# Optimization experiments

Measured on AMD Instinct MI355X. Metric: run time of the kernel, lower is better.

Reference implementation:

```python
import jax, jax.numpy as jnp
import numpy as np

DIM = 1024
HEADS = 16
HEAD_DIM = DIM // HEADS
SCALE = HEAD_DIM ** -0.5


def apply_rope(x, theta=10000.0):
    # x: [b, h, n, d]
    n, d = x.shape[2], x.shape[3]
    seq = jnp.arange(n, dtype=jnp.float32)
    inv = 1.0 / (theta ** (jnp.arange(0, d, 2, dtype=jnp.float32) / d))  # [d/2]
    freqs = seq[:, None] * inv[None, :]  # [n, d/2]
    cos = jnp.cos(freqs)[None, None]  # [1,1,n,d/2]
    sin = jnp.sin(freqs)[None, None]
    x1, x2 = jnp.split(x, 2, axis=-1)
    return jnp.concatenate([x1 * cos - x2 * sin, x1 * sin + x2 * cos], axis=-1)


def setup_inputs() -> dict:
    key = jax.random.key(0)
    ks = jax.random.split(key, 7)
    s = DIM ** -0.5
    return {
        "x": jax.random.normal(ks[0], (2, 2048, DIM), dtype=jnp.float32),
        "Wqkv": jax.random.normal(ks[1], (3 * DIM, DIM), dtype=jnp.float32) * s,
        "bqkv": jax.random.normal(ks[2], (3 * DIM,), dtype=jnp.float32) * 0.02,
        "Wpre": jax.random.normal(ks[3], (HEADS, HEADS), dtype=jnp.float32) * HEADS ** -0.5,
        "Wpost": jax.random.normal(ks[4], (HEADS, HEADS), dtype=jnp.float32) * HEADS ** -0.5,
        "Wout": jax.random.normal(ks[5], (DIM, DIM), dtype=jnp.float32) * s,
        "bout": jax.random.normal(ks[6], (DIM,), dtype=jnp.float32) * 0.02,
    }


def reference(x, Wqkv, bqkv, Wpre, Wpost, Wout, bout):
    b, n, _ = x.shape
    qkv = x @ Wqkv.T + bqkv  # [b, n, 3*dim]
    q, k, v = jnp.split(qkv, 3, axis=-1)
    # [b, n, dim] -> [b, h, n, d]
    reshape = lambda t: t.reshape(b, n, HEADS, HEAD_DIM).transpose(0, 2, 1, 3)
    q, k, v = reshape(q), reshape(k), reshape(v)
    q = apply_rope(q)
    k = apply_rope(k)
    logits = jnp.einsum('bhid,bhjd->bhij', q, k) * SCALE
    # pre-softmax talking heads: Linear(heads->heads), y[...,g] = sum_h x[...,h] * Wpre[g,h]
    logits = jnp.einsum('bhij,gh->bgij', logits, Wpre)
    attn = jax.nn.softmax(logits, axis=-1)
    attn = jnp.einsum('bhij,gh->bgij', attn, Wpost)
    out = jnp.einsum('bhij,bhjd->bhid', attn, v)
    out = out.transpose(0, 2, 1, 3).reshape(b, n, DIM)
    return out @ Wout.T + bout
```

## Files before the change

### kernel.cpp

```cpp
#include <hip/hip_runtime.h>
#include <cstddef>
#include <cstdint>

#define SEQ    2048
#define DMODEL 1024
#define NHEAD  16
#define HDIM   64
#define SCALE  0.125f
#define LOG2E  1.4426950408889634f

typedef _Float16 f16;
typedef unsigned short u16;
typedef unsigned int   u32;
typedef __attribute__((ext_vector_type(8))) _Float16 h8v;
typedef __attribute__((ext_vector_type(4))) _Float16 h4v;
typedef __attribute__((ext_vector_type(4))) float    f4v;

__device__ __forceinline__ u32 pkh(float a, float b) {
    u16 x = __builtin_bit_cast(u16, (f16)a);
    u16 y = __builtin_bit_cast(u16, (f16)b);
    return (u32)x | ((u32)y << 16);
}

__device__ __forceinline__ float fexp2(float x) {
#if __has_builtin(__builtin_amdgcn_exp2f)
    return __builtin_amdgcn_exp2f(x);
#else
    return exp2f(x);
#endif
}

__device__ __forceinline__ f4v mfma32(h8v a, h8v b, f4v c) {
    return __builtin_amdgcn_mfma_f32_16x16x32_f16(a, b, c, 0, 0, 0);
}
__device__ __forceinline__ f4v mfma16(h4v a, h4v b, f4v c) {
    return __builtin_amdgcn_mfma_f32_16x16x16f16(a, b, c, 0, 0, 0);
}

__global__ __launch_bounds__(256)
void rope_tab_kernel(float2* __restrict__ tab)
{
    int gid = blockIdx.x * 256 + threadIdx.x;
    int pos = gid >> 5, t = gid & 31;
    float inv = exp2f((float)(-2 * t) * (0.015625f * 13.287712379549449f));
    float c, s;
    sincosf((float)pos * inv, &s, &c);
    tab[gid] = make_float2(c, s);
}

__global__ __launch_bounds__(256)
void cvt_f16_kernel(const float* __restrict__ x, const float* __restrict__ Wqkv,
                    const float* __restrict__ Wout,
                    f16* __restrict__ Xh, f16* __restrict__ Wqh, f16* __restrict__ Woh)
{
    size_t i = ((size_t)blockIdx.x * 256 + threadIdx.x) * 8;
    const float* src; f16* dst; size_t off;
    if (i < 4194304)      { src = x;    dst = Xh;  off = i; }
    else if (i < 7340032) { src = Wqkv; dst = Wqh; off = i - 4194304; }
    else                  { src = Wout; dst = Woh; off = i - 7340032; }
    float4 a = *(const float4*)&src[off];
    float4 b = *(const float4*)&src[off + 4];
    uint4 o;
    o.x = pkh(a.x, a.y); o.y = pkh(a.z, a.w);
    o.z = pkh(b.x, b.y); o.w = pkh(b.z, b.w);
    *(uint4*)&dst[off] = o;
}

__global__ __launch_bounds__(256)
void gemm_f16_kernel(const f16* __restrict__ A, const f16* __restrict__ B,
                     const float* __restrict__ bias, void* __restrict__ Cout,
                     int N, int K, int mode)
{
    __shared__ __align__(16) char Asb[8192];
    __shared__ __align__(16) char Bsb[8192];
    int tid = threadIdx.x;
    int w = tid >> 6, l = tid & 63, lr = l & 15, lc = l >> 4;
    int row0 = blockIdx.y * 128, col0 = blockIdx.x * 128;
    int wr = (w >> 1) * 64, wc = (w & 1) * 64;

    f4v acc[4][4];
    #pragma unroll
    for (int m = 0; m < 4; ++m)
        #pragma unroll
        for (int n = 0; n < 4; ++n) acc[m][n] = (f4v){0.f, 0.f, 0.f, 0.f};

    int r0 = tid >> 2, k0s = tid & 3;
    int r1 = (tid + 256) >> 2, k1s = tid & 3;

    uint4 ra0, ra1, rb0, rb1;
    ra0 = *(const uint4*)&A[(size_t)(row0 + r0) * K + k0s * 8];
    ra1 = *(const uint4*)&A[(size_t)(row0 + r1) * K + k1s * 8];
    rb0 = *(const uint4*)&B[(size_t)(col0 + r0) * K + k0s * 8];
    rb1 = *(const uint4*)&B[(size_t)(col0 + r1) * K + k1s * 8];

    int NT = K >> 5;
    for (int kt = 0; kt < NT; ++kt) {
        *(uint4*)(Asb + r0 * 64 + ((k0s ^ (r0 & 3)) << 4)) = ra0;
        *(uint4*)(Asb + r1 * 64 + ((k1s ^ (r1 & 3)) << 4)) = ra1;
        *(uint4*)(Bsb + r0 * 64 + ((k0s ^ (r0 & 3)) << 4)) = rb0;
        *(uint4*)(Bsb + r1 * 64 + ((k1s ^ (r1 & 3)) << 4)) = rb1;
        if (kt + 1 < NT) {
            int kk = (kt + 1) * 32;
            ra0 = *(const uint4*)&A[(size_t)(row0 + r0) * K + kk + k0s * 8];
            ra1 = *(const uint4*)&A[(size_t)(row0 + r1) * K + kk + k1s * 8];
            rb0 = *(const uint4*)&B[(size_t)(col0 + r0) * K + kk + k0s * 8];
            rb1 = *(const uint4*)&B[(size_t)(col0 + r1) * K + kk + k1s * 8];
        }
        __syncthreads();
        h8v af[4], bf[4];
        #pragma unroll
        for (int m = 0; m < 4; ++m) {
            int row = wr + m * 16 + lr;
            af[m] = *(h8v*)(Asb + row * 64 + ((lc ^ (row & 3)) << 4));
        }
        #pragma unroll
        for (int n = 0; n < 4; ++n) {
            int col = wc + n * 16 + lr;
            bf[n] = *(h8v*)(Bsb + col * 64 + ((lc ^ (col & 3)) << 4));
        }
        #pragma unroll
        for (int m = 0; m < 4; ++m)
            #pragma unroll
            for (int n = 0; n < 4; ++n)
                acc[m][n] = mfma32(af[m], bf[n], acc[m][n]);
        __syncthreads();
    }

    #pragma unroll
    for (int m = 0; m < 4; ++m)
        #pragma unroll
        for (int r = 0; r < 4; ++r) {
            int row = row0 + wr + m * 16 + lc * 4 + r;
            #pragma unroll
            for (int n = 0; n < 4; ++n) {
                int col = col0 + wc + n * 16 + lr;
                float v = acc[m][n][r] + bias[col];
                if (mode == 0) ((f16*)Cout)[(size_t)row * N + col] = (f16)v;
                else           ((float*)Cout)[(size_t)row * N + col] = v;
            }
        }
}

__global__ __launch_bounds__(256)
void pack_qk_kernel(const f16* __restrict__ QKVh, const float2* __restrict__ tab,
                    f16* __restrict__ Qh, f16* __restrict__ Kh)
{
    int gid = blockIdx.x * 256 + threadIdx.x;
    int i     = gid & 15;
    int t8    = (gid >> 4) & 3;
    int h     = (gid >> 6) & 15;
    int rh    = (gid >> 10) & 255;
    int which = (gid >> 18) & 1;
    int row = rh * 16 + i;
    int pos = row & (SEQ - 1);
    int b   = row >> 11;
    f16* dst = which ? Kh : Qh;

    h8v x1 = *(const h8v*)&QKVh[(size_t)row * 3072 + which * 1024 + h * 64 + t8 * 8];
    h8v x2 = *(const h8v*)&QKVh[(size_t)row * 3072 + which * 1024 + h * 64 + t8 * 8 + 32];

    float y1[8], y2[8];
    #pragma unroll
    for (int e = 0; e < 8; ++e) {
        int t = t8 * 8 + e;
        float2 cs = tab[pos * 32 + t];
        float a1 = (float)x1[e], a2 = (float)x2[e];
        y1[e] = a1 * cs.x - a2 * cs.y;
        y2[e] = a1 * cs.y + a2 * cs.x;
    }
    int it = pos >> 4;
    size_t b0 = (((((size_t)(b*128 + it)*16 + h)*2 + 0)*4 + t8)*16 + i)*8;
    size_t b1 = (((((size_t)(b*128 + it)*16 + h)*2 + 1)*4 + t8)*16 + i)*8;
    uint4 o0, o1;
    o0.x = pkh(y1[0], y1[1]); o0.y = pkh(y1[2], y1[3]);
    o0.z = pkh(y1[4], y1[5]); o0.w = pkh(y1[6], y1[7]);
    o1.x = pkh(y2[0], y2[1]); o1.y = pkh(y2[2], y2[3]);
    o1.z = pkh(y2[4], y2[5]); o1.w = pkh(y2[6], y2[7]);
    *(uint4*)(dst + b0) = o0;
    *(uint4*)(dst + b1) = o1;
}

__global__ __launch_bounds__(256)
void pack_v_kernel(const f16* __restrict__ QKVh, f16* __restrict__ Vt)
{
    int gid = blockIdx.x * 256 + threadIdx.x;
    int dd = gid & 15;
    int jc = (gid >> 4) & 3;
    int dt = (gid >> 6) & 3;
    int g  = (gid >> 8) & 15;
    int jt = (gid >> 12) & 63;
    int b  = (gid >> 18) & 1;
    int d = g * 64 + dt * 16 + dd;
    f16 v[8];
    #pragma unroll
    for (int e = 0; e < 8; ++e) {
        int j = jt * 32 + jc * 8 + e;
        v[e] = QKVh[(size_t)(b * SEQ + j) * 3072 + 2048 + d];
    }
    size_t off = ((((((size_t)b*64 + jt)*16 + g)*4 + dt)*4 + jc)*16 + dd)*8;
    uint4 o;
    o.x = pkh((float)v[0], (float)v[1]); o.y = pkh((float)v[2], (float)v[3]);
    o.z = pkh((float)v[4], (float)v[5]); o.w = pkh((float)v[6], (float)v[7]);
    *(uint4*)(Vt + off) = o;
}

__global__ __launch_bounds__(256)
void pack_ctx_kernel(const f16* __restrict__ Cp, f16* __restrict__ Ch)
{
    size_t i = ((size_t)blockIdx.x * 256 + threadIdx.x) * 8;
    h8v p0 = *(const h8v*)&Cp[i];
    h8v p1 = *(const h8v*)&Cp[i + 4194304];
    float s[8];
    #pragma unroll
    for (int e = 0; e < 8; ++e)
        s[e] = (float)p0[e] + (float)p1[e];
    uint4 o;
    o.x = pkh(s[0], s[1]); o.y = pkh(s[2], s[3]);
    o.z = pkh(s[4], s[5]); o.w = pkh(s[6], s[7]);
    *(uint4*)&Ch[i] = o;
}

template<int FULL>
__global__ __launch_bounds__(1024, FULL ? 1 : 2)
void attn_core(const f16* __restrict__ Qh, const f16* __restrict__ Kh,
               const f16* __restrict__ Vt, const float* __restrict__ Wpre,
               const float* __restrict__ Wpost, const float* __restrict__ Zp,
               float* __restrict__ Zout, f16* __restrict__ Octx)
{
    __shared__ __align__(16) char ss[65536];
    __shared__ __align__(16) char es[FULL ? 65536 : 16];

    int tid = threadIdx.x;
    int wv = tid >> 6;
    int l  = tid & 63;
    int lr = l & 15;
    int lc = l >> 4;

    int bid   = blockIdx.x;
    int it2   = bid & 63;
    int b     = (bid >> 6) & 1;
    int split = bid >> 7;

    h4v wpre4;
    #pragma unroll
    for (int e = 0; e < 4; ++e) wpre4[e] = (f16)(Wpre[lr * 16 + lc * 4 + e] * (SCALE * LOG2E));
    h4v wpost;
    if (FULL) {
        #pragma unroll
        for (int e = 0; e < 4; ++e) wpost[e] = (f16)Wpost[lr * 16 + lc * 4 + e];
    }

    h8v qf[2][2];
    #pragma unroll
    for (int itl = 0; itl < 2; ++itl)
        #pragma unroll
        for (int ks = 0; ks < 2; ++ks) {
            size_t off = ((((size_t)((b*128 + it2*2 + itl)*16 + wv)*2 + ks)*4 + lc)*16 + lr)*8;
            qf[itl][ks] = *(const h8v*)(Qh + off);
        }

    f4v m4n[2];
    if (FULL) {
        float* zrd = (float*)ss;
        if (tid < 512) {
            int itl = tid >> 8, g = (tid >> 4) & 15, i = tid & 15;
            size_t idx = (size_t)(b * 16 + g) * SEQ + it2 * 32 + itl * 16 + i;
            zrd[tid] = log2f(Zp[idx] + Zp[65536 + idx] + Zp[131072 + idx] + Zp[196608 + idx]);
        }
        __syncthreads();
        #pragma unroll
        for (int itl = 0; itl < 2; ++itl)
            #pragma unroll
            for (int r = 0; r < 4; ++r)
                m4n[itl][r] = -zrd[itl * 256 + (lc * 4 + r) * 16 + lr];
        __syncthreads();
    }

    f4v pv[2][4];
    if (FULL) {
        #pragma unroll
        for (int itl = 0; itl < 2; ++itl)
            #pragma unroll
            for (int dt = 0; dt < 4; ++dt) pv[itl][dt] = (f4v){0.f, 0.f, 0.f, 0.f};
    }
    float zacc[2][4] = {};

    const int NSTEP = FULL ? 16 : 8;
    int j0beg = split * (FULL ? 1024 : 512);
    int jtbeg = j0beg >> 4;
    int jvbeg = j0beg >> 5;

    for (int s = 0; s < NSTEP; ++s) {
        h8v vf0[4];
        if (FULL) {
            int jt32 = jvbeg + s * 2;
            #pragma unroll
            for (int dt = 0; dt < 4; ++dt) {
                size_t voff = (((((size_t)(b*64 + jt32)*16 + wv)*4 + dt)*4 + lc)*16 + lr)*8;
                vf0[dt] = *(const h8v*)(Vt + voff);
            }
        }
        #pragma unroll
        for (int jsp = 0; jsp < 2; ++jsp) {
            h8v kf[2][2];
            #pragma unroll
            for (int js2 = 0; js2 < 2; ++js2)
                #pragma unroll
                for (int ks = 0; ks < 2; ++ks) {
                    int jt = jtbeg + s * 4 + jsp * 2 + js2;
                    size_t off = ((((size_t)((b*128 + jt)*16 + wv)*2 + ks)*4 + lc)*16 + lr)*8;
                    kf[js2][ks] = *(const h8v*)(Kh + off);
                }
            #pragma unroll
            for (int itl = 0; itl < 2; ++itl)
                #pragma unroll
                for (int js2 = 0; js2 < 2; ++js2) {
                    f4v q = (f4v){0.f, 0.f, 0.f, 0.f};
                    q = mfma32(qf[itl][0], kf[js2][0], q);
                    q = mfma32(qf[itl][1], kf[js2][1], q);
                    int js = jsp * 2 + js2;
                    #pragma unroll
                    for (int r = 0; r < 4; ++r) {
                        int i = lc * 4 + r;
                        int addr = itl * 32768 + ((wv >> 2) * 4 + js) * 2048
                                 + i * 128 + ((lr ^ i) << 3) + (wv & 3) * 2;
                        *(u16*)(ss + addr) = __builtin_bit_cast(u16, (f16)q[r]);
                    }
                }
        }
        __syncthreads();

        #pragma unroll
        for (int itl = 0; itl < 2; ++itl) {
            u32 a2p[4][2];
            #pragma unroll
            for (int tt = 0; tt < 4; ++tt) {
                int t = wv * 4 + tt;
                int addr = itl * 32768 + (lc * 4 + (t >> 4)) * 2048
                         + lr * 128 + (((t & 15) ^ lr) << 3);
                union { uint2 u; h4v v; } cv;
                cv.u = *(uint2*)(ss + addr);
                if (!FULL) {
                    f4v s1 = mfma16(wpre4, cv.v, (f4v){0.f, 0.f, 0.f, 0.f});
                    #pragma unroll
                    for (int r = 0; r < 4; ++r) zacc[itl][r] += fexp2(s1[r]);
                } else {
                    f4v s1 = mfma16(wpre4, cv.v, m4n[itl]);
                    h4v pf;
                    #pragma unroll
                    for (int r = 0; r < 4; ++r) pf[r] = (f16)fexp2(s1[r]);
                    f4v a2 = mfma16(wpost, pf, (f4v){0.f, 0.f, 0.f, 0.f});
                    #pragma unroll
                    for (int r = 0; r < 4; ++r) {
                        u32 v = (u32)__builtin_bit_cast(u16, (f16)a2[r]);
                        if (tt & 1) a2p[r][tt >> 1] |= v << 16;
                        else        a2p[r][tt >> 1]  = v;
                    }
                }
            }
            if (FULL) {
                #pragma unroll
                for (int r = 0; r < 4; ++r) {
                    int gq = lc * 4 + r;
                    int off = itl * 32768 + gq * 2048 + lr * 128
                            + ((wv * 8) ^ ((lr & 7) << 4));
                    *(uint2*)(es + off) = make_uint2(a2p[r][0], a2p[r][1]);
                }
            }
        }
        h8v vf1[4];
        if (FULL) {
            int jt32 = jvbeg + s * 2 + 1;
            #pragma unroll
            for (int dt = 0; dt < 4; ++dt) {
                size_t voff = (((((size_t)(b*64 + jt32)*16 + wv)*4 + dt)*4 + lc)*16 + lr)*8;
                vf1[dt] = *(const h8v*)(Vt + voff);
            }
        }
        __syncthreads();

        if (FULL) {
            #pragma unroll
            for (int itl = 0; itl < 2; ++itl) {
                h8v af0 = *(h8v*)(es + itl * 32768 + wv * 2048 + lr * 128
                                  + ((0 * 64 + lc * 16) ^ ((lr & 7) << 4)));
                h8v af1 = *(h8v*)(es + itl * 32768 + wv * 2048 + lr * 128
                                  + ((1 * 64 + lc * 16) ^ ((lr & 7) << 4)));
                #pragma unroll
                for (int dt = 0; dt < 4; ++dt)
                    pv[itl][dt] = mfma32(af0, vf0[dt], pv[itl][dt]);
                #pragma unroll
                for (int dt = 0; dt < 4; ++dt)
                    pv[itl][dt] = mfma32(af1, vf1[dt], pv[itl][dt]);
            }
        }
    }

    if (!FULL) {
        float* zrd = (float*)ss;
        #pragma unroll
        for (int itl = 0; itl < 2; ++itl)
            #pragma unroll
            for (int r = 0; r < 4; ++r)
                zrd[itl * 4096 + ((lc * 4 + r) * 16 + lr) * 16 + wv] = zacc[itl][r];
        __syncthreads();
        if (tid < 512) {
            int itl = tid >> 8, gi = tid & 255;
            float z = 0.f;
            #pragma unroll
            for (int w2 = 0; w2 < 16; ++w2) z += zrd[itl * 4096 + gi * 16 + w2];
            int g = gi >> 4, i = gi & 15;
            Zout[(size_t)split * 65536 + (size_t)(b * 16 + g) * SEQ + it2 * 32 + itl * 16 + i] = z;
        }
    } else {
        f16* dst = Octx + (size_t)split * 4194304;
        #pragma unroll
        for (int itl = 0; itl < 2; ++itl)
            #pragma unroll
            for (int dt = 0; dt < 4; ++dt)
                #pragma unroll
                for (int r = 0; r < 4; ++r) {
                    int row = it2 * 32 + itl * 16 + lc * 4 + r;
                    int col = wv * 64 + dt * 16 + lr;
                    dst[(size_t)(b * SEQ + row) * DMODEL + col] = (f16)pv[itl][dt][r];
                }
    }
}

extern "C" void kernel_launch(void* const* d_in, const int* in_sizes, int n_in,
                              void* d_out, int out_size, void* d_ws, size_t ws_size,
                              hipStream_t stream)
{
    const float* x     = (const float*)d_in[0];
    const float* Wqkv  = (const float*)d_in[1];
    const float* bqkv  = (const float*)d_in[2];
    const float* Wpre  = (const float*)d_in[3];
    const float* Wpost = (const float*)d_in[4];
    const float* Wout  = (const float*)d_in[5];
    const float* bout  = (const float*)d_in[6];
    float* out = (float*)d_out;

    float* ws = (float*)d_ws;
    f16*   QKVh = (f16*)(ws);
    f16*   CTXp = (f16*)(ws);
    f16*   Xh   = (f16*)(ws + 8388608);
    f16*   Wqh  = (f16*)(ws + 10485760);
    f16*   Woh  = (f16*)(ws + 12058624);
    f16*   Qh   = (f16*)(ws + 12582912);
    f16*   Kh   = (f16*)(ws + 14680064);
    f16*   Vt   = (f16*)(ws + 16777216);
    f16*   Ch   = (f16*)(ws + 18874368);
    float* Zp   = ws + 19922944;
    float2* Tab = (float2*)(ws + 20185088);

    dim3 blk(256);
    rope_tab_kernel<<<256, blk, 0, stream>>>(Tab);
    cvt_f16_kernel<<<4096, blk, 0, stream>>>(x, Wqkv, Wout, Xh, Wqh, Woh);
    gemm_f16_kernel<<<dim3(24, 32), blk, 0, stream>>>(Xh, Wqh, bqkv, (void*)QKVh, 3072, 1024, 0);
    pack_qk_kernel<<<2048, blk, 0, stream>>>(QKVh, Tab, Qh, Kh);
    pack_v_kernel<<<2048, blk, 0, stream>>>(QKVh, Vt);
    attn_core<0><<<512, dim3(1024), 0, stream>>>(Qh, Kh, Vt, Wpre, Wpost, nullptr, Zp, nullptr);
    attn_core<1><<<256, dim3(1024), 0, stream>>>(Qh, Kh, Vt, Wpre, Wpost, Zp, nullptr, CTXp);
    pack_ctx_kernel<<<2048, blk, 0, stream>>>(CTXp, Ch);
    gemm_f16_kernel<<<dim3(8, 32), blk, 0, stream>>>(Ch, Woh, bout, (void*)out, 1024, 1024, 1);
}
```

Before: 209.5 us.

## Use direct global-to-LDS loads in GEMM and prefetch K fragments in attention

The GEMM now uses global_load_lds to stream A/B tiles straight into shared memory, replacing the register-staged load-and-store path, and issues the next tile's loads after the second barrier. The attention kernel loads the second half of the K fragments before computing scores and, in the full pass, prefetches the next step's first K fragments across the barrier. The aim is to hide global load latency and cut register and VGPR-to-LDS traffic. The GEMM loses its register double buffering, so next-tile loads now land during the barrier rather than overlapping the MFMA loop, and the LDS layout depends on how global_load_lds places each wave's 64 lanes.

```diff
diff --git a/kernel.cpp b/kernel.cpp
--- a/kernel.cpp
+++ b/kernel.cpp
@@ -36,6 +36,10 @@
 __device__ __forceinline__ f4v mfma16(h4v a, h4v b, f4v c) {
     return __builtin_amdgcn_mfma_f32_16x16x16f16(a, b, c, 0, 0, 0);
 }
+
+#define GLD16(src, dst) __builtin_amdgcn_global_load_lds(                    \
+        (const __attribute__((address_space(1))) void*)(src),                \
+        (__attribute__((address_space(3))) void*)(dst), 16, 0, 0)
 
 __global__ __launch_bounds__(256)
 void rope_tab_kernel(float2* __restrict__ tab)
@@ -84,28 +88,25 @@
         #pragma unroll
         for (int n = 0; n < 4; ++n) acc[m][n] = (f4v){0.f, 0.f, 0.f, 0.f};
 
-    int r0 = tid >> 2, k0s = tid & 3;
-    int r1 = (tid + 256) >> 2, k1s = tid & 3;
-
-    uint4 ra0, ra1, rb0, rb1;
-    ra0 = *(const uint4*)&A[(size_t)(row0 + r0) * K + k0s * 8];
-    ra1 = *(const uint4*)&A[(size_t)(row0 + r1) * K + k1s * 8];
-    rb0 = *(const uint4*)&B[(size_t)(col0 + r0) * K + k0s * 8];
-    rb1 = *(const uint4*)&B[(size_t)(col0 + r1) * K + k1s * 8];
+    int r0 = tid >> 2;
+    int k0 = (tid & 3) ^ (r0 & 3);
+    int r1 = (tid + 256) >> 2;
+    int k1 = (tid & 3) ^ (r1 & 3);
+    char* lA0 = Asb + w * 1024;
+    char* lA1 = Asb + 4096 + w * 1024;
+    char* lB0 = Bsb + w * 1024;
+    char* lB1 = Bsb + 4096 + w * 1024;
+
+    const f16* pa0 = &A[(size_t)(row0 + r0) * K + k0 * 8];
+    const f16* pa1 = &A[(size_t)(row0 + r1) * K + k1 * 8];
+    const f16* pb0 = &B[(size_t)(col0 + r0) * K + k0 * 8];
+    const f16* pb1 = &B[(size_t)(col0 + r1) * K + k1 * 8];
+
+    GLD16(pa0, lA0); GLD16(pa1, lA1);
+    GLD16(pb0, lB0); GLD16(pb1, lB1);
 
     int NT = K >> 5;
     for (int kt = 0; kt < NT; ++kt) {
-        *(uint4*)(Asb + r0 * 64 + ((k0s ^ (r0 & 3)) << 4)) = ra0;
-        *(uint4*)(Asb + r1 * 64 + ((k1s ^ (r1 & 3)) << 4)) = ra1;
-        *(uint4*)(Bsb + r0 * 64 + ((k0s ^ (r0 & 3)) << 4)) = rb0;
-        *(uint4*)(Bsb + r1 * 64 + ((k1s ^ (r1 & 3)) << 4)) = rb1;
-        if (kt + 1 < NT) {
-            int kk = (kt + 1) * 32;
-            ra0 = *(const uint4*)&A[(size_t)(row0 + r0) * K + kk + k0s * 8];
-            ra1 = *(const uint4*)&A[(size_t)(row0 + r1) * K + kk + k1s * 8];
-            rb0 = *(const uint4*)&B[(size_t)(col0 + r0) * K + kk + k0s * 8];
-            rb1 = *(const uint4*)&B[(size_t)(col0 + r1) * K + kk + k1s * 8];
-        }
         __syncthreads();
         h8v af[4], bf[4];
         #pragma unroll
@@ -124,6 +125,11 @@
             for (int n = 0; n < 4; ++n)
                 acc[m][n] = mfma32(af[m], bf[n], acc[m][n]);
         __syncthreads();
+        if (kt + 1 < NT) {
+            int kk = (kt + 1) * 32;
+            GLD16(pa0 + kk, lA0); GLD16(pa1 + kk, lA1);
+            GLD16(pb0 + kk, lB0); GLD16(pb1 + kk, lB1);
+        }
     }
 
     #pragma unroll
@@ -290,7 +296,22 @@
     int jtbeg = j0beg >> 4;
     int jvbeg = j0beg >> 5;
 
+    auto ldK2 = [&](int s, int jsp, h8v (&kf)[2][2]) {
+        #pragma unroll
+        for (int js2 = 0; js2 < 2; ++js2)
+            #pragma unroll
+            for (int ks = 0; ks < 2; ++ks) {
+                int jt = jtbeg + s * 4 + jsp * 2 + js2;
+                size_t off = ((((size_t)((b*128 + jt)*16 + wv)*2 + ks)*4 + lc)*16 + lr)*8;
+                kf[js2][ks] = *(const h8v*)(Kh + off);
+            }
+    };
+
+    h8v kp[2][2];
+    if (FULL) ldK2(0, 0, kp);
+
     for (int s = 0; s < NSTEP; ++s) {
+        if (!FULL) ldK2(s, 0, kp);
         h8v vf0[4];
         if (FULL) {
             int jt32 = jvbeg + s * 2;
@@ -300,24 +321,19 @@
                 vf0[dt] = *(const h8v*)(Vt + voff);
             }
         }
+        h8v kf1[2][2];
+        ldK2(s, 1, kf1);
+
         #pragma unroll
         for (int jsp = 0; jsp < 2; ++jsp) {
-            h8v kf[2][2];
-            #pragma unroll
-            for (int js2 = 0; js2 < 2; ++js2)
-                #pragma unroll
-                for (int ks = 0; ks < 2; ++ks) {
-                    int jt = jtbeg + s * 4 + jsp * 2 + js2;
-                    size_t off = ((((size_t)((b*128 + jt)*16 + wv)*2 + ks)*4 + lc)*16 + lr)*8;
-                    kf[js2][ks] = *(const h8v*)(Kh + off);
-                }
             #pragma unroll
             for (int itl = 0; itl < 2; ++itl)
                 #pragma unroll
                 for (int js2 = 0; js2 < 2; ++js2) {
+                    const h8v* kk = jsp ? kf1[js2] : kp[js2];
                     f4v q = (f4v){0.f, 0.f, 0.f, 0.f};
-                    q = mfma32(qf[itl][0], kf[js2][0], q);
-                    q = mfma32(qf[itl][1], kf[js2][1], q);
+                    q = mfma32(qf[itl][0], kk[0], q);
+                    q = mfma32(qf[itl][1], kk[1], q);
                     int js = jsp * 2 + js2;
                     #pragma unroll
                     for (int r = 0; r < 4; ++r) {
@@ -328,6 +344,7 @@
                     }
                 }
         }
+        if (FULL && s + 1 < NSTEP) ldK2(s + 1, 0, kp);
         __syncthreads();
 
         #pragma unroll
```

After: 277.9 us. 32.6% more time.
